# Performance work log

Measured on AMD Instinct MI355X. Metric: run time of the kernel, lower is better.

## Reference

```python
import jax, jax.numpy as jnp
import numpy as np

N = 100000   # nodes
E = 1600000  # edges
F_IN = 64    # n_features
H = 32       # hidden_size
OUT = 1      # output_size


def _lin(k, fan_in, fan_out):
    return (jax.random.normal(k, (fan_in, fan_out), jnp.float32) / np.sqrt(fan_in)).astype(jnp.float32)


def setup_inputs() -> dict:
    key = jax.random.key(0)
    ks = jax.random.split(key, 16)
    x = jax.random.normal(ks[0], (N, F_IN), jnp.float32)
    edge_index = jax.random.randint(ks[1], (2, E), 0, N, dtype=jnp.int64)
    # guarantee current_node (=0) has outgoing edges so the legal-move mask is non-empty
    edge_index = edge_index.at[0, :64].set(0)
    edge_attr = jax.random.uniform(ks[2], (E,), jnp.float32)
    return {
        "x": x, "edge_index": edge_index, "edge_attr": edge_attr, "current_node": 0,
        # conv_in: GraphConv(F_IN -> H)
        "Win_rel": _lin(ks[3], F_IN, H), "bin_rel": jnp.zeros((H,), jnp.float32), "Win_root": _lin(ks[4], F_IN, H),
        # conv_hidden: GraphConv(H -> H)
        "Wh_rel": _lin(ks[5], H, H), "bh_rel": jnp.zeros((H,), jnp.float32), "Wh_root": _lin(ks[6], H, H),
        # policy_conv: GraphConv(H -> OUT)
        "Wp_rel": _lin(ks[7], H, OUT), "bp_rel": jnp.zeros((OUT,), jnp.float32), "Wp_root": _lin(ks[8], H, OUT),
        # value_conv: GraphConv(H -> OUT)
        "Wv_rel": _lin(ks[9], H, OUT), "bv_rel": jnp.zeros((OUT,), jnp.float32), "Wv_root": _lin(ks[10], H, OUT),
    }


def _graph_conv(h, src, dst, ew, W_rel, b_rel, W_root):
    # PyG GraphConv: out_i = W_root h_i + W_rel * sum_{j->i} e_ji * h_j + b
    msg = h[src] * ew[:, None]                              # [E, d] gather + scale
    agg = jax.ops.segment_sum(msg, dst, num_segments=N)      # [N, d] scatter-add
    return agg @ W_rel + b_rel + h @ W_root


def reference(x, edge_index, edge_attr, current_node,
              Win_rel, bin_rel, Win_root,
              Wh_rel, bh_rel, Wh_root,
              Wp_rel, bp_rel, Wp_root,
              Wv_rel, bv_rel, Wv_root):
    src, dst = edge_index[0], edge_index[1]
    h = jax.nn.relu(_graph_conv(x, src, dst, edge_attr, Win_rel, bin_rel, Win_root))
    h = jax.nn.relu(_graph_conv(h, src, dst, edge_attr, Wh_rel, bh_rel, Wh_root))
    p = _graph_conv(h, src, dst, edge_attr, Wp_rel, bp_rel, Wp_root)  # [N, 1]
    v = _graph_conv(h, src, dst, edge_attr, Wv_rel, bv_rel, Wv_root)  # [N, 1]
    # illegal_moves_mask: 1 for nodes directly reachable from current_node
    hit = (src == current_node).astype(jnp.float32)
    mask = (jnp.zeros((N,), jnp.float32).at[dst].add(hit) > 0).astype(jnp.float32)
    p_m = mask * p.T                                   # [1, N]
    p_m = jnp.where(p_m == 0, -jnp.inf, p_m)
    p_soft = jax.nn.softmax(p_m, axis=1)
    v_m = mask * v.T                                   # [1, N]
    return p_soft.reshape(-1), v_m.reshape(-1)
```

## Files before the change

### kernel.cpp

```cpp
#include <hip/hip_runtime.h>
#include <hip/hip_fp16.h>
#include <cmath>

static constexpr int NN = 100000;
static constexpr int NE = 1600000;
static const size_t NW = (size_t)NN * 32;
static constexpr int SUB = 256;
static constexpr int NSUB = 391;
static constexpr int CH = 8192;
static constexpr int NCH = (NE + CH - 1) / CH;
static constexpr int BCAP = 5200;
static constexpr int MCAP = 4096;

__device__ __forceinline__ float ent_w(unsigned e)
{
    return __half2float(__ushort_as_half((unsigned short)(e >> 17)));
}
__device__ __forceinline__ int ent_s(unsigned e)
{
    int s = (int)(e & 0x1FFFF);
    return s < NN ? s : NN - 1;
}

__device__ __forceinline__ float4 pack8(const float* v)
{
    union { __half2 h2[4]; float4 f4; } u;
    u.h2[0] = __floats2half2_rn(v[0], v[1]);
    u.h2[1] = __floats2half2_rn(v[2], v[3]);
    u.h2[2] = __floats2half2_rn(v[4], v[5]);
    u.h2[3] = __floats2half2_rn(v[6], v[7]);
    return u.f4;
}

__global__ void __launch_bounds__(512) countC_k(
    const int* __restrict__ src, const int* __restrict__ dst,
    const int* __restrict__ curp, int* __restrict__ maskb,
    int* __restrict__ mcount, int* __restrict__ mlist,
    int* __restrict__ blkcnt)
{
    __shared__ int lhist[NSUB];
    int t = threadIdx.x;
    for (int i = t; i < NSUB; i += 512) lhist[i] = 0;
    __syncthreads();
    int c0 = blockIdx.x * CH;
    int cur = curp[0];
#pragma unroll
    for (int it = 0; it < CH / 512; ++it) {
        int e = c0 + it * 512 + t;
        if (e < NE) {
            int d = dst[e];
            if ((unsigned)d < (unsigned)NN) {
                atomicAdd(&lhist[d >> 8], 1);
                if (src[e] == cur) {
                    if (atomicExch(maskb + d, 1) == 0) {
                        int idx = atomicAdd(mcount, 1);
                        if (idx < MCAP) mlist[idx] = d;
                    }
                }
            }
        }
    }
    __syncthreads();
    for (int b = t; b < NSUB; b += 512)
        blkcnt[b * NCH + blockIdx.x] = lhist[b];
}

__global__ void __launch_bounds__(256) scan_blk_k(
    const int* __restrict__ blkcnt, int* __restrict__ blkbase,
    int* __restrict__ btot)
{
    __shared__ int tmp[256];
    int b = blockIdx.x, t = threadIdx.x;
    int v = (t < NCH) ? blkcnt[b * NCH + t] : 0;
    tmp[t] = v;
    __syncthreads();
    for (int s = 1; s < 256; s <<= 1) {
        int x = tmp[t];
        int a = (t >= s) ? tmp[t - s] : 0;
        __syncthreads();
        tmp[t] = x + a;
        __syncthreads();
    }
    if (t < NCH) blkbase[b * NCH + t] = tmp[t] - v;
    if (t == 255) btot[b] = tmp[255];
}

__global__ void __launch_bounds__(512) scan_btot_k(
    const int* __restrict__ btot, int* __restrict__ gbase)
{
    __shared__ int tmp[512];
    int t = threadIdx.x;
    int v = (t < NSUB) ? btot[t] : 0;
    tmp[t] = v;
    __syncthreads();
    for (int s = 1; s < 512; s <<= 1) {
        int x = tmp[t];
        int a = (t >= s) ? tmp[t - s] : 0;
        __syncthreads();
        tmp[t] = x + a;
        __syncthreads();
    }
    if (t < NSUB) gbase[t] = tmp[t] - v;
}

__global__ void __launch_bounds__(512) writeC_k(
    const int* __restrict__ src, const int* __restrict__ dst,
    const float* __restrict__ ew, const int* __restrict__ blkbase,
    uint2* __restrict__ buckets)
{
    __shared__ uint2 sBuf[CH];
    __shared__ int lhist[NSUB];
    __shared__ int lpos[NSUB];
    __shared__ int lstart[NSUB];
    __shared__ int lbase[NSUB];
    __shared__ int tscan[512];
    int t = threadIdx.x;
    for (int i = t; i < NSUB; i += 512) { lhist[i] = 0; lpos[i] = 0; }
    __syncthreads();
    int c0 = blockIdx.x * CH;
    uint2 rent[CH / 512];
    int rb[CH / 512];
#pragma unroll
    for (int it = 0; it < CH / 512; ++it) {
        int e = c0 + it * 512 + t;
        rb[it] = -1;
        if (e < NE) {
            int d = dst[e];
            if ((unsigned)d < (unsigned)NN) {
                rb[it] = d >> 8;
                unsigned bits = __half_as_ushort(__float2half(ew[e]));
                rent[it].x = ((unsigned)src[e] & 0x1FFFF) | (bits << 17);
                rent[it].y = (unsigned)d;
                atomicAdd(&lhist[rb[it]], 1);
            }
        }
    }
    __syncthreads();
    int v = (t < NSUB) ? lhist[t] : 0;
    tscan[t] = v;
    __syncthreads();
    for (int s = 1; s < 512; s <<= 1) {
        int x = tscan[t];
        int a = (t >= s) ? tscan[t - s] : 0;
        __syncthreads();
        tscan[t] = x + a;
        __syncthreads();
    }
    if (t < NSUB) {
        lstart[t] = tscan[t] - v;
        lbase[t] = blkbase[t * NCH + blockIdx.x];
    }
    __syncthreads();
#pragma unroll
    for (int it = 0; it < CH / 512; ++it) {
        if (rb[it] >= 0) {
            int p = atomicAdd(&lpos[rb[it]], 1);
            sBuf[lstart[rb[it]] + p] = rent[it];
        }
    }
    __syncthreads();
    int total = lstart[NSUB - 1] + lhist[NSUB - 1];
    for (int j = t; j < total; j += 512) {
        uint2 e = sBuf[j];
        int b = (int)(e.y >> 8);
        if (b >= NSUB) b = NSUB - 1;
        unsigned pos = (unsigned)(lbase[b] + (j - lstart[b]));
        if (pos < (unsigned)BCAP) buckets[(size_t)b * BCAP + pos] = e;
    }
}

__global__ void __launch_bounds__(512) sortB_k(
    const uint2* __restrict__ buckets, const int* __restrict__ btot,
    const int* __restrict__ gbase, unsigned* __restrict__ csr4,
    int* __restrict__ deg, int* __restrict__ off)
{
    __shared__ uint2 sBuf[BCAP];
    __shared__ int lhist[SUB];
    __shared__ int lstart[SUB];
    __shared__ int lcur[SUB];
    __shared__ int tscan[256];
    int g = blockIdx.x, t = threadIdx.x;
    if (t < SUB) { lhist[t] = 0; lcur[t] = 0; }
    __syncthreads();
    int cnt = btot[g];
    if (cnt < 0) cnt = 0;
    if (cnt > BCAP) cnt = BCAP;
    const uint2* bk = buckets + (size_t)g * BCAP;
    for (int i = t; i < cnt; i += 512) {
        uint2 e = bk[i];
        sBuf[i] = e;
        atomicAdd(&lhist[e.y & (SUB - 1)], 1);
    }
    __syncthreads();
    if (t < 256) tscan[t] = lhist[t];
    __syncthreads();
    for (int s = 1; s < 256; s <<= 1) {
        int x = 0, a = 0;
        if (t < 256) { x = tscan[t]; a = (t >= s) ? tscan[t - s] : 0; }
        __syncthreads();
        if (t < 256) tscan[t] = x + a;
        __syncthreads();
    }
    if (t < 256) lstart[t] = tscan[t] - lhist[t];
    __syncthreads();
    int base = gbase[g];
    for (int i = t; i < cnt; i += 512) {
        uint2 e = sBuf[i];
        int ld = (int)(e.y & (SUB - 1));
        int p = atomicAdd(&lcur[ld], 1);
        unsigned pos = (unsigned)(base + lstart[ld] + p);
        if (pos < (unsigned)NE) csr4[pos] = e.x;
    }
    if (t < SUB) {
        int n = g * SUB + t;
        if (n < NN) {
            deg[n] = lhist[t];
            off[n] = base + lstart[t];
        }
    }
}

__global__ void __launch_bounds__(256) mm1_k(
    const float* __restrict__ x, const float* __restrict__ Wrel,
    const float* __restrict__ Wroot, const float* __restrict__ bin,
    __half* __restrict__ proj1, __half* __restrict__ root1)
{
    __shared__ float sX[128 * 65];
    __shared__ float sW[64 * 68];
    int t = threadIdx.x;
    for (int i = t; i < 64 * 32; i += 256) {
        int k = i >> 5, j = i & 31;
        sW[k * 68 + j] = Wrel[i];
        sW[k * 68 + 32 + j] = Wroot[i];
    }
    int base = blockIdx.x * 128;
    for (int i = t; i < 2048; i += 256) {
        int node = i >> 4;
        int k = (i & 15) * 4;
        int n = base + node;
        if (n >= NN) n = NN - 1;
        float4 v = *(const float4*)(x + (size_t)n * 64 + k);
        float* p = sX + node * 65 + k;
        p[0] = v.x; p[1] = v.y; p[2] = v.z; p[3] = v.w;
    }
    __syncthreads();
    int cg = t & 7;
    int ng = t >> 3;
    int c0 = 8 * cg;
    float acc[4][8] = {};
    for (int k = 0; k < 64; ++k) {
        float xv0 = sX[(4 * ng + 0) * 65 + k];
        float xv1 = sX[(4 * ng + 1) * 65 + k];
        float xv2 = sX[(4 * ng + 2) * 65 + k];
        float xv3 = sX[(4 * ng + 3) * 65 + k];
        float4 w0 = *(const float4*)(sW + k * 68 + c0);
        float4 w1 = *(const float4*)(sW + k * 68 + c0 + 4);
        const float* wp = (const float*)&w0;
#pragma unroll
        for (int j = 0; j < 4; ++j) {
            float w = wp[j];
            acc[0][j] = fmaf(xv0, w, acc[0][j]);
            acc[1][j] = fmaf(xv1, w, acc[1][j]);
            acc[2][j] = fmaf(xv2, w, acc[2][j]);
            acc[3][j] = fmaf(xv3, w, acc[3][j]);
        }
        const float* wq = (const float*)&w1;
#pragma unroll
        for (int j = 0; j < 4; ++j) {
            float w = wq[j];
            acc[0][4 + j] = fmaf(xv0, w, acc[0][4 + j]);
            acc[1][4 + j] = fmaf(xv1, w, acc[1][4 + j]);
            acc[2][4 + j] = fmaf(xv2, w, acc[2][4 + j]);
            acc[3][4 + j] = fmaf(xv3, w, acc[3][4 + j]);
        }
    }
#pragma unroll
    for (int r = 0; r < 4; ++r) {
        int n = base + 4 * ng + r;
        if (n >= NN) break;
        if (cg < 4) {
            *(float4*)(proj1 + (size_t)n * 32 + c0) = pack8(acc[r]);
        } else {
            int c = c0 - 32;
            float v[8];
#pragma unroll
            for (int j = 0; j < 8; ++j) v[j] = acc[r][j] + bin[c + j];
            *(float4*)(root1 + (size_t)n * 32 + c) = pack8(v);
        }
    }
}

__global__ void __launch_bounds__(256) mm2_k(
    const __half* __restrict__ h1, const float* __restrict__ Wrel,
    const float* __restrict__ Wroot, const float* __restrict__ bh,
    __half* __restrict__ proj2, __half* __restrict__ root2)
{
    __shared__ float sX[128 * 33];
    __shared__ float sW[32 * 68];
    int t = threadIdx.x;
    for (int i = t; i < 32 * 32; i += 256) {
        int k = i >> 5, j = i & 31;
        sW[k * 68 + j] = Wrel[i];
        sW[k * 68 + 32 + j] = Wroot[i];
    }
    int base = blockIdx.x * 128;
    for (int i = t; i < 512; i += 256) {
        int node = i >> 2;
        int hs = (i & 3) * 8;
        int n = base + node;
        if (n >= NN) n = NN - 1;
        float4 v = *(const float4*)(h1 + (size_t)n * 32 + hs);
        const __half2* hp = (const __half2*)&v;
        float* p = sX + node * 33 + hs;
#pragma unroll
        for (int u = 0; u < 4; ++u) {
            float2 f2 = __half22float2(hp[u]);
            p[2 * u] = f2.x;
            p[2 * u + 1] = f2.y;
        }
    }
    __syncthreads();
    int cg = t & 7;
    int ng = t >> 3;
    int c0 = 8 * cg;
    float acc[4][8] = {};
    for (int k = 0; k < 32; ++k) {
        float xv0 = sX[(4 * ng + 0) * 33 + k];
        float xv1 = sX[(4 * ng + 1) * 33 + k];
        float xv2 = sX[(4 * ng + 2) * 33 + k];
        float xv3 = sX[(4 * ng + 3) * 33 + k];
        float4 w0 = *(const float4*)(sW + k * 68 + c0);
        float4 w1 = *(const float4*)(sW + k * 68 + c0 + 4);
        const float* wp = (const float*)&w0;
#pragma unroll
        for (int j = 0; j < 4; ++j) {
            float w = wp[j];
            acc[0][j] = fmaf(xv0, w, acc[0][j]);
            acc[1][j] = fmaf(xv1, w, acc[1][j]);
            acc[2][j] = fmaf(xv2, w, acc[2][j]);
            acc[3][j] = fmaf(xv3, w, acc[3][j]);
        }
        const float* wq = (const float*)&w1;
#pragma unroll
        for (int j = 0; j < 4; ++j) {
            float w = wq[j];
            acc[0][4 + j] = fmaf(xv0, w, acc[0][4 + j]);
            acc[1][4 + j] = fmaf(xv1, w, acc[1][4 + j]);
            acc[2][4 + j] = fmaf(xv2, w, acc[2][4 + j]);
            acc[3][4 + j] = fmaf(xv3, w, acc[3][4 + j]);
        }
    }
#pragma unroll
    for (int r = 0; r < 4; ++r) {
        int n = base + 4 * ng + r;
        if (n >= NN) break;
        if (cg < 4) {
            *(float4*)(proj2 + (size_t)n * 32 + c0) = pack8(acc[r]);
        } else {
            int c = c0 - 32;
            float v[8];
#pragma unroll
            for (int j = 0; j < 8; ++j) v[j] = acc[r][j] + bh[c + j];
            *(float4*)(root2 + (size_t)n * 32 + c) = pack8(v);
        }
    }
}

__global__ void __launch_bounds__(256) agg1_v4(
    const __half* __restrict__ proj1, const __half* __restrict__ root1,
    const unsigned* __restrict__ csr4, const int* __restrict__ off,
    const int* __restrict__ deg, __half* __restrict__ h1)
{
    int t = threadIdx.x;
    int q = t & 3;
    int f0 = q * 8;
    int n = blockIdx.x * 64 + (t >> 2);
    if (n >= NN) return;
    int st = off[n];
    int dg = deg[n];
    if (st < 0) st = 0;
    if (st > NE) st = NE;
    if (dg < 0) dg = 0;
    if (dg > NE - st) dg = NE - st;
    float acc[8] = {0.f, 0.f, 0.f, 0.f, 0.f, 0.f, 0.f, 0.f};
    int i = 0;
    for (; i + 1 < dg; i += 2) {
        unsigned e0 = csr4[st + i];
        unsigned e1 = csr4[st + i + 1];
        float w0 = ent_w(e0), w1 = ent_w(e1);
        float4 r0 = *(const float4*)(proj1 + (size_t)ent_s(e0) * 32 + f0);
        float4 r1 = *(const float4*)(proj1 + (size_t)ent_s(e1) * 32 + f0);
        const __half2* h0 = (const __half2*)&r0;
        const __half2* h1p = (const __half2*)&r1;
#pragma unroll
        for (int u = 0; u < 4; ++u) {
            float2 a = __half22float2(h0[u]);
            float2 b = __half22float2(h1p[u]);
            acc[2 * u] = fmaf(w0, a.x, acc[2 * u]);
            acc[2 * u + 1] = fmaf(w0, a.y, acc[2 * u + 1]);
            acc[2 * u] = fmaf(w1, b.x, acc[2 * u]);
            acc[2 * u + 1] = fmaf(w1, b.y, acc[2 * u + 1]);
        }
    }
    if (i < dg) {
        unsigned e0 = csr4[st + i];
        float w0 = ent_w(e0);
        float4 r0 = *(const float4*)(proj1 + (size_t)ent_s(e0) * 32 + f0);
        const __half2* h0 = (const __half2*)&r0;
#pragma unroll
        for (int u = 0; u < 4; ++u) {
            float2 a = __half22float2(h0[u]);
            acc[2 * u] = fmaf(w0, a.x, acc[2 * u]);
            acc[2 * u + 1] = fmaf(w0, a.y, acc[2 * u + 1]);
        }
    }
    float4 rr = *(const float4*)(root1 + (size_t)n * 32 + f0);
    const __half2* rp = (const __half2*)&rr;
    float h[8];
#pragma unroll
    for (int u = 0; u < 4; ++u) {
        float2 f2 = __half22float2(rp[u]);
        h[2 * u] = fmaxf(acc[2 * u] + f2.x, 0.f);
        h[2 * u + 1] = fmaxf(acc[2 * u + 1] + f2.y, 0.f);
    }
    *(float4*)(h1 + (size_t)n * 32 + f0) = pack8(h);
}

__global__ void __launch_bounds__(256) agg2_v4(
    const __half* __restrict__ proj2, const __half* __restrict__ root2,
    const float* __restrict__ Wp_rel, const float* __restrict__ Wp_root,
    const float* __restrict__ bp, const float* __restrict__ Wv_rel,
    const float* __restrict__ Wv_root, const float* __restrict__ bv,
    const unsigned* __restrict__ csr4, const int* __restrict__ off,
    const int* __restrict__ deg, float2* __restrict__ pv,
    float* __restrict__ pbase, float* __restrict__ vbase)
{
    __shared__ float sHead[4 * 32];
    if (threadIdx.x < 32) {
        sHead[threadIdx.x] = Wp_rel[threadIdx.x];
        sHead[32 + threadIdx.x] = Wp_root[threadIdx.x];
        sHead[64 + threadIdx.x] = Wv_rel[threadIdx.x];
        sHead[96 + threadIdx.x] = Wv_root[threadIdx.x];
    }
    __syncthreads();
    int t = threadIdx.x;
    int q = t & 3;
    int f0 = q * 8;
    int n = blockIdx.x * 64 + (t >> 2);
    if (n >= NN) return;
    int st = off[n];
    int dg = deg[n];
    if (st < 0) st = 0;
    if (st > NE) st = NE;
    if (dg < 0) dg = 0;
    if (dg > NE - st) dg = NE - st;
    float acc[8] = {0.f, 0.f, 0.f, 0.f, 0.f, 0.f, 0.f, 0.f};
    int i = 0;
    for (; i + 1 < dg; i += 2) {
        unsigned e0 = csr4[st + i];
        unsigned e1 = csr4[st + i + 1];
        float w0 = ent_w(e0), w1 = ent_w(e1);
        float4 r0 = *(const float4*)(proj2 + (size_t)ent_s(e0) * 32 + f0);
        float4 r1 = *(const float4*)(proj2 + (size_t)ent_s(e1) * 32 + f0);
        const __half2* h0 = (const __half2*)&r0;
        const __half2* h1p = (const __half2*)&r1;
#pragma unroll
        for (int u = 0; u < 4; ++u) {
            float2 a = __half22float2(h0[u]);
            float2 b = __half22float2(h1p[u]);
            acc[2 * u] = fmaf(w0, a.x, acc[2 * u]);
            acc[2 * u + 1] = fmaf(w0, a.y, acc[2 * u + 1]);
            acc[2 * u] = fmaf(w1, b.x, acc[2 * u]);
            acc[2 * u + 1] = fmaf(w1, b.y, acc[2 * u + 1]);
        }
    }
    if (i < dg) {
        unsigned e0 = csr4[st + i];
        float w0 = ent_w(e0);
        float4 r0 = *(const float4*)(proj2 + (size_t)ent_s(e0) * 32 + f0);
        const __half2* h0 = (const __half2*)&r0;
#pragma unroll
        for (int u = 0; u < 4; ++u) {
            float2 a = __half22float2(h0[u]);
            acc[2 * u] = fmaf(w0, a.x, acc[2 * u]);
            acc[2 * u + 1] = fmaf(w0, a.y, acc[2 * u + 1]);
        }
    }
    float4 rr = *(const float4*)(root2 + (size_t)n * 32 + f0);
    const __half2* rp = (const __half2*)&rr;
    float h[8];
#pragma unroll
    for (int u = 0; u < 4; ++u) {
        float2 f2 = __half22float2(rp[u]);
        h[2 * u] = fmaxf(acc[2 * u] + f2.x, 0.f);
        h[2 * u + 1] = fmaxf(acc[2 * u + 1] + f2.y, 0.f);
    }
    float prv = 0.f, pov = 0.f, vrv = 0.f, vov = 0.f;
#pragma unroll
    for (int j = 0; j < 8; ++j) {
        prv = fmaf(h[j], sHead[f0 + j], prv);
        pov = fmaf(h[j], sHead[32 + f0 + j], pov);
        vrv = fmaf(h[j], sHead[64 + f0 + j], vrv);
        vov = fmaf(h[j], sHead[96 + f0 + j], vov);
    }
#pragma unroll
    for (int m = 1; m <= 2; m <<= 1) {
        prv += __shfl_xor(prv, m, 64);
        pov += __shfl_xor(pov, m, 64);
        vrv += __shfl_xor(vrv, m, 64);
        vov += __shfl_xor(vov, m, 64);
    }
    if (q == 0) {
        pv[n] = make_float2(prv, vrv);
        pbase[n] = pov + bp[0];
        vbase[n] = vov + bv[0];
    }
}

__global__ void __launch_bounds__(256) masked_softmax_k(
    const int* __restrict__ mlist, const int* __restrict__ mcount,
    const unsigned* __restrict__ csr4, const int* __restrict__ off,
    const int* __restrict__ deg, const float2* __restrict__ pv,
    const float* __restrict__ pbase, const float* __restrict__ vbase,
    float* __restrict__ out_p, float* __restrict__ out_v)
{
    __shared__ float sPm[MCAP];
    __shared__ float sV[MCAP];
    __shared__ int sN[MCAP];
    __shared__ float sMx, sSum;
    __shared__ float sred[4];
    int m = mcount[0];
    if (m > MCAP) m = MCAP;
    if (m < 0) m = 0;
    for (int idx = threadIdx.x; idx < m; idx += 256) {
        int n = mlist[idx];
        if ((unsigned)n >= (unsigned)NN) n = 0;
        sN[idx] = n;
        int st = off[n];
        int dg = deg[n];
        if (st < 0) st = 0;
        if (st > NE) st = NE;
        if (dg < 0) dg = 0;
        if (dg > NE - st) dg = NE - st;
        float pa = 0.f, va = 0.f;
        for (int i = 0; i < dg; ++i) {
            unsigned ent = csr4[st + i];
            int s = ent_s(ent);
            float w = ent_w(ent);
            float2 tv = pv[s];
            pa = fmaf(tv.x, w, pa);
            va = fmaf(tv.y, w, va);
        }
        float p = pa + pbase[n];
        sPm[idx] = (p == 0.f) ? -INFINITY : p;
        sV[idx] = va + vbase[n];
    }
    __syncthreads();
    float mx = -INFINITY;
    for (int i = threadIdx.x; i < m; i += 256) mx = fmaxf(mx, sPm[i]);
#pragma unroll
    for (int k = 32; k; k >>= 1) mx = fmaxf(mx, __shfl_xor(mx, k, 64));
    if ((threadIdx.x & 63) == 0) sred[threadIdx.x >> 6] = mx;
    __syncthreads();
    if (threadIdx.x == 0)
        sMx = fmaxf(fmaxf(sred[0], sred[1]), fmaxf(sred[2], sred[3]));
    __syncthreads();
    float sum = 0.f;
    for (int i = threadIdx.x; i < m; i += 256) {
        float x = sPm[i];
        sum += (x == -INFINITY) ? 0.f : expf(x - sMx);
    }
#pragma unroll
    for (int k = 32; k; k >>= 1) sum += __shfl_xor(sum, k, 64);
    if ((threadIdx.x & 63) == 0) sred[threadIdx.x >> 6] = sum;
    __syncthreads();
    if (threadIdx.x == 0) sSum = sred[0] + sred[1] + sred[2] + sred[3];
    __syncthreads();
    for (int idx = threadIdx.x; idx < m; idx += 256) {
        int n = sN[idx];
        float x = sPm[idx];
        out_p[n] = (x == -INFINITY) ? 0.f : expf(x - sMx) / sSum;
        out_v[n] = sV[idx];
    }
}

extern "C" void kernel_launch(void* const* d_in, const int* in_sizes, int n_in,
                              void* d_out, int out_size, void* d_ws,
                              size_t ws_size, hipStream_t stream)
{
    const float* x        = (const float*)d_in[0];
    const int*   ei       = (const int*)d_in[1];
    const float* ew       = (const float*)d_in[2];
    const int*   cur      = (const int*)d_in[3];
    const float* Win_rel  = (const float*)d_in[4];
    const float* bin_rel  = (const float*)d_in[5];
    const float* Win_root = (const float*)d_in[6];
    const float* Wh_rel   = (const float*)d_in[7];
    const float* bh_rel   = (const float*)d_in[8];
    const float* Wh_root  = (const float*)d_in[9];
    const float* Wp_rel   = (const float*)d_in[10];
    const float* bp       = (const float*)d_in[11];
    const float* Wp_root  = (const float*)d_in[12];
    const float* Wv_rel   = (const float*)d_in[13];
    const float* bv       = (const float*)d_in[14];
    const float* Wv_root  = (const float*)d_in[15];

    const int* srcA = ei;
    const int* dstA = ei + NE;

    char* w8 = (char*)d_ws;
    unsigned* csr4 = (unsigned*)w8;
    int* deg    = (int*)(csr4 + NE);
    int* off    = deg + NN;
    int* maskb  = off + NN;
    int* mcount = maskb + NN;
    int* mlist  = mcount + 8;
    int* btot   = mlist + MCAP;
    int* gbase  = btot + 400;
    __half* proj1 = (__half*)(gbase + 400);
    __half* root1 = proj1 + NW;
    __half* h1    = root1 + NW;
    __half* proj2 = h1 + NW;
    __half* root2 = proj2 + NW;
    float2* pv    = (float2*)(root2 + NW);
    float* pbase  = (float*)(pv + NN);
    float* vbase  = pbase + NN;
    uint2* buckets = (uint2*)proj1;
    int* blkcnt  = (int*)(buckets + (size_t)NSUB * BCAP);
    int* blkbase = blkcnt + NSUB * NCH;

    float* out_p = (float*)d_out;
    float* out_v = out_p + NN;

    const int NB_MM  = (NN + 127) / 128;
    const int NB_AGG = (NN + 63) / 64;

    hipMemsetAsync(maskb, 0, ((size_t)NN + 8) * sizeof(int), stream);
    hipMemsetAsync(d_out, 0, 2 * (size_t)NN * sizeof(float), stream);

    countC_k<<<NCH, 512, 0, stream>>>(srcA, dstA, cur, maskb, mcount, mlist,
                                      blkcnt);
    scan_blk_k<<<NSUB, 256, 0, stream>>>(blkcnt, blkbase, btot);
    scan_btot_k<<<1, 512, 0, stream>>>(btot, gbase);
    writeC_k<<<NCH, 512, 0, stream>>>(srcA, dstA, ew, blkbase, buckets);
    sortB_k<<<NSUB, 512, 0, stream>>>(buckets, btot, gbase, csr4, deg, off);

    mm1_k<<<NB_MM, 256, 0, stream>>>(x, Win_rel, Win_root, bin_rel, proj1,
                                     root1);
    agg1_v4<<<NB_AGG, 256, 0, stream>>>(proj1, root1, csr4, off, deg, h1);
    mm2_k<<<NB_MM, 256, 0, stream>>>(h1, Wh_rel, Wh_root, bh_rel, proj2, root2);
    agg2_v4<<<NB_AGG, 256, 0, stream>>>(proj2, root2, Wp_rel, Wp_root, bp,
                                        Wv_rel, Wv_root, bv, csr4, off, deg,
                                        pv, pbase, vbase);
    masked_softmax_k<<<1, 256, 0, stream>>>(mlist, mcount, csr4, off, deg, pv,
                                            pbase, vbase, out_p, out_v);
}
```

Measured before the change: 263.0 us.

## Fuse CSR build passes with first projection GEMM into one kernel

Replaces the separate count, two scan, and write passes with a single pass. Each chunk reserves space inside fixed-capacity per-bucket slots through global atomics, so the CSR is laid out at bucket*BCAP offsets instead of being compactly prefix-summed. The same launch also runs the first projection GEMM in extra blocks that share the LDS through a union, overlapping compute with the edge bucketing. The output memset is folded into agg2's stores. This removes several launches and one full read of the edge arrays. In exchange, bucket order now depends on atomic timing (nondeterministic edge order within a node), and the GEMM blocks run at 512 threads with fewer rows per thread.

```diff
diff --git a/kernel.cpp b/kernel.cpp
--- a/kernel.cpp
+++ b/kernel.cpp
@@ -10,6 +10,7 @@
 static constexpr int CH = 8192;
 static constexpr int NCH = (NE + CH - 1) / CH;
 static constexpr int BCAP = 5200;
+static constexpr int CSRN = NSUB * BCAP;
 static constexpr int MCAP = 4096;
 
 __device__ __forceinline__ float ent_w(unsigned e)
@@ -32,147 +33,156 @@
     return u.f4;
 }
 
-__global__ void __launch_bounds__(512) countC_k(
+__global__ void __launch_bounds__(512) fused_build_mm1_k(
     const int* __restrict__ src, const int* __restrict__ dst,
-    const int* __restrict__ curp, int* __restrict__ maskb,
-    int* __restrict__ mcount, int* __restrict__ mlist,
-    int* __restrict__ blkcnt)
-{
-    __shared__ int lhist[NSUB];
+    const float* __restrict__ ew, const int* __restrict__ curp,
+    int* __restrict__ maskb, int* __restrict__ mcount, int* __restrict__ mlist,
+    int* __restrict__ bcnt, uint2* __restrict__ buckets,
+    const float* __restrict__ x, const float* __restrict__ Wrel,
+    const float* __restrict__ Wroot, const float* __restrict__ bin,
+    __half* __restrict__ proj1, __half* __restrict__ root1)
+{
+    __shared__ union {
+        struct {
+            uint2 sBuf[CH];
+            int lhist[NSUB];
+            int lpos[NSUB];
+            int lstart[NSUB];
+            int lbase[NSUB];
+            int tscan[512];
+        } s;
+        struct {
+            float sX[128 * 65];
+            float sW[64 * 68];
+        } m;
+    } u;
+
     int t = threadIdx.x;
-    for (int i = t; i < NSUB; i += 512) lhist[i] = 0;
-    __syncthreads();
-    int c0 = blockIdx.x * CH;
-    int cur = curp[0];
-#pragma unroll
-    for (int it = 0; it < CH / 512; ++it) {
-        int e = c0 + it * 512 + t;
-        if (e < NE) {
-            int d = dst[e];
-            if ((unsigned)d < (unsigned)NN) {
-                atomicAdd(&lhist[d >> 8], 1);
-                if (src[e] == cur) {
-                    if (atomicExch(maskb + d, 1) == 0) {
-                        int idx = atomicAdd(mcount, 1);
-                        if (idx < MCAP) mlist[idx] = d;
+    int bid = blockIdx.x;
+
+    if (bid < NCH) {
+        for (int i = t; i < NSUB; i += 512) { u.s.lhist[i] = 0; u.s.lpos[i] = 0; }
+        __syncthreads();
+        int c0 = bid * CH;
+        int cur = curp[0];
+        uint2 rent[CH / 512];
+        int rb[CH / 512];
+#pragma unroll
+        for (int it = 0; it < CH / 512; ++it) {
+            int e = c0 + it * 512 + t;
+            rb[it] = -1;
+            if (e < NE) {
+                int d = dst[e];
+                int sv = src[e];
+                if ((unsigned)d < (unsigned)NN) {
+                    rb[it] = d >> 8;
+                    unsigned bits = __half_as_ushort(__float2half(ew[e]));
+                    rent[it].x = ((unsigned)sv & 0x1FFFF) | (bits << 17);
+                    rent[it].y = (unsigned)d;
+                    atomicAdd(&u.s.lhist[rb[it]], 1);
+                    if (sv == cur) {
+                        if (atomicExch(maskb + d, 1) == 0) {
+                            int idx = atomicAdd(mcount, 1);
+                            if (idx < MCAP) mlist[idx] = d;
+                        }
                     }
                 }
             }
         }
-    }
-    __syncthreads();
-    for (int b = t; b < NSUB; b += 512)
-        blkcnt[b * NCH + blockIdx.x] = lhist[b];
-}
-
-__global__ void __launch_bounds__(256) scan_blk_k(
-    const int* __restrict__ blkcnt, int* __restrict__ blkbase,
-    int* __restrict__ btot)
-{
-    __shared__ int tmp[256];
-    int b = blockIdx.x, t = threadIdx.x;
-    int v = (t < NCH) ? blkcnt[b * NCH + t] : 0;
-    tmp[t] = v;
-    __syncthreads();
-    for (int s = 1; s < 256; s <<= 1) {
-        int x = tmp[t];
-        int a = (t >= s) ? tmp[t - s] : 0;
-        __syncthreads();
-        tmp[t] = x + a;
-        __syncthreads();
-    }
-    if (t < NCH) blkbase[b * NCH + t] = tmp[t] - v;
-    if (t == 255) btot[b] = tmp[255];
-}
-
-__global__ void __launch_bounds__(512) scan_btot_k(
-    const int* __restrict__ btot, int* __restrict__ gbase)
-{
-    __shared__ int tmp[512];
-    int t = threadIdx.x;
-    int v = (t < NSUB) ? btot[t] : 0;
-    tmp[t] = v;
-    __syncthreads();
-    for (int s = 1; s < 512; s <<= 1) {
-        int x = tmp[t];
-        int a = (t >= s) ? tmp[t - s] : 0;
-        __syncthreads();
-        tmp[t] = x + a;
-        __syncthreads();
-    }
-    if (t < NSUB) gbase[t] = tmp[t] - v;
-}
-
-__global__ void __launch_bounds__(512) writeC_k(
-    const int* __restrict__ src, const int* __restrict__ dst,
-    const float* __restrict__ ew, const int* __restrict__ blkbase,
-    uint2* __restrict__ buckets)
-{
-    __shared__ uint2 sBuf[CH];
-    __shared__ int lhist[NSUB];
-    __shared__ int lpos[NSUB];
-    __shared__ int lstart[NSUB];
-    __shared__ int lbase[NSUB];
-    __shared__ int tscan[512];
-    int t = threadIdx.x;
-    for (int i = t; i < NSUB; i += 512) { lhist[i] = 0; lpos[i] = 0; }
-    __syncthreads();
-    int c0 = blockIdx.x * CH;
-    uint2 rent[CH / 512];
-    int rb[CH / 512];
-#pragma unroll
-    for (int it = 0; it < CH / 512; ++it) {
-        int e = c0 + it * 512 + t;
-        rb[it] = -1;
-        if (e < NE) {
-            int d = dst[e];
-            if ((unsigned)d < (unsigned)NN) {
-                rb[it] = d >> 8;
-                unsigned bits = __half_as_ushort(__float2half(ew[e]));
-                rent[it].x = ((unsigned)src[e] & 0x1FFFF) | (bits << 17);
-                rent[it].y = (unsigned)d;
-                atomicAdd(&lhist[rb[it]], 1);
+        __syncthreads();
+        int v = (t < NSUB) ? u.s.lhist[t] : 0;
+        u.s.tscan[t] = v;
+        __syncthreads();
+        for (int sh = 1; sh < 512; sh <<= 1) {
+            int xv = u.s.tscan[t];
+            int a = (t >= sh) ? u.s.tscan[t - sh] : 0;
+            __syncthreads();
+            u.s.tscan[t] = xv + a;
+            __syncthreads();
+        }
+        if (t < NSUB) {
+            u.s.lstart[t] = u.s.tscan[t] - v;
+            u.s.lbase[t] = (v > 0) ? atomicAdd(&bcnt[t], v) : 0;
+        }
+        __syncthreads();
+#pragma unroll
+        for (int it = 0; it < CH / 512; ++it) {
+            if (rb[it] >= 0) {
+                int p = atomicAdd(&u.s.lpos[rb[it]], 1);
+                u.s.sBuf[u.s.lstart[rb[it]] + p] = rent[it];
             }
         }
-    }
-    __syncthreads();
-    int v = (t < NSUB) ? lhist[t] : 0;
-    tscan[t] = v;
-    __syncthreads();
-    for (int s = 1; s < 512; s <<= 1) {
-        int x = tscan[t];
-        int a = (t >= s) ? tscan[t - s] : 0;
-        __syncthreads();
-        tscan[t] = x + a;
-        __syncthreads();
-    }
-    if (t < NSUB) {
-        lstart[t] = tscan[t] - v;
-        lbase[t] = blkbase[t * NCH + blockIdx.x];
-    }
-    __syncthreads();
-#pragma unroll
-    for (int it = 0; it < CH / 512; ++it) {
-        if (rb[it] >= 0) {
-            int p = atomicAdd(&lpos[rb[it]], 1);
-            sBuf[lstart[rb[it]] + p] = rent[it];
-        }
-    }
-    __syncthreads();
-    int total = lstart[NSUB - 1] + lhist[NSUB - 1];
-    for (int j = t; j < total; j += 512) {
-        uint2 e = sBuf[j];
-        int b = (int)(e.y >> 8);
-        if (b >= NSUB) b = NSUB - 1;
-        unsigned pos = (unsigned)(lbase[b] + (j - lstart[b]));
-        if (pos < (unsigned)BCAP) buckets[(size_t)b * BCAP + pos] = e;
+        __syncthreads();
+        int total = u.s.lstart[NSUB - 1] + u.s.lhist[NSUB - 1];
+        for (int j = t; j < total; j += 512) {
+            uint2 en = u.s.sBuf[j];
+            int b = (int)(en.y >> 8);
+            if (b >= NSUB) b = NSUB - 1;
+            unsigned pos = (unsigned)(u.s.lbase[b] + (j - u.s.lstart[b]));
+            if (pos < (unsigned)BCAP) buckets[(size_t)b * BCAP + pos] = en;
+        }
+    } else {
+        int mb = bid - NCH;
+        for (int i = t; i < 64 * 32; i += 512) {
+            int k = i >> 5, j = i & 31;
+            u.m.sW[k * 68 + j] = Wrel[i];
+            u.m.sW[k * 68 + 32 + j] = Wroot[i];
+        }
+        int base = mb * 128;
+        for (int i = t; i < 2048; i += 512) {
+            int node = i >> 4;
+            int k = (i & 15) * 4;
+            int n = base + node;
+            if (n >= NN) n = NN - 1;
+            float4 v4 = *(const float4*)(x + (size_t)n * 64 + k);
+            float* p = u.m.sX + node * 65 + k;
+            p[0] = v4.x; p[1] = v4.y; p[2] = v4.z; p[3] = v4.w;
+        }
+        __syncthreads();
+        int cg = t & 7;
+        int ng = t >> 3;
+        int c0m = 8 * cg;
+        float acc[2][8] = {};
+        for (int k = 0; k < 64; ++k) {
+            float xv0 = u.m.sX[(2 * ng + 0) * 65 + k];
+            float xv1 = u.m.sX[(2 * ng + 1) * 65 + k];
+            float4 w0 = *(const float4*)(u.m.sW + k * 68 + c0m);
+            float4 w1 = *(const float4*)(u.m.sW + k * 68 + c0m + 4);
+            const float* wp = (const float*)&w0;
+#pragma unroll
+            for (int j = 0; j < 4; ++j) {
+                float w = wp[j];
+                acc[0][j] = fmaf(xv0, w, acc[0][j]);
+                acc[1][j] = fmaf(xv1, w, acc[1][j]);
+            }
+            const float* wq = (const float*)&w1;
+#pragma unroll
+            for (int j = 0; j < 4; ++j) {
+                float w = wq[j];
+                acc[0][4 + j] = fmaf(xv0, w, acc[0][4 + j]);
+                acc[1][4 + j] = fmaf(xv1, w, acc[1][4 + j]);
+            }
+        }
+#pragma unroll
+        for (int r = 0; r < 2; ++r) {
+            int n = base + 2 * ng + r;
+            if (n >= NN) break;
+            if (cg < 4) {
+                *(float4*)(proj1 + (size_t)n * 32 + c0m) = pack8(acc[r]);
+            } else {
+                int c = c0m - 32;
+                float vv[8];
+#pragma unroll
+                for (int j = 0; j < 8; ++j) vv[j] = acc[r][j] + bin[c + j];
+                *(float4*)(root1 + (size_t)n * 32 + c) = pack8(vv);
+            }
+        }
     }
 }
 
 __global__ void __launch_bounds__(512) sortB_k(
-    const uint2* __restrict__ buckets, const int* __restrict__ btot,
-    const int* __restrict__ gbase, unsigned* __restrict__ csr4,
-    int* __restrict__ deg, int* __restrict__ off)
+    const uint2* __restrict__ buckets, const int* __restrict__ bcnt,
+    unsigned* __restrict__ csr4, int* __restrict__ deg, int* __restrict__ off)
 {
     __shared__ uint2 sBuf[BCAP];
     __shared__ int lhist[SUB];
@@ -182,7 +192,7 @@
     int g = blockIdx.x, t = threadIdx.x;
     if (t < SUB) { lhist[t] = 0; lcur[t] = 0; }
     __syncthreads();
-    int cnt = btot[g];
+    int cnt = bcnt[g];
     if (cnt < 0) cnt = 0;
     if (cnt > BCAP) cnt = BCAP;
     const uint2* bk = buckets + (size_t)g * BCAP;
@@ -203,89 +213,19 @@
     }
     if (t < 256) lstart[t] = tscan[t] - lhist[t];
     __syncthreads();
-    int base = gbase[g];
+    int base = g * BCAP;
     for (int i = t; i < cnt; i += 512) {
         uint2 e = sBuf[i];
         int ld = (int)(e.y & (SUB - 1));
         int p = atomicAdd(&lcur[ld], 1);
         unsigned pos = (unsigned)(base + lstart[ld] + p);
-        if (pos < (unsigned)NE) csr4[pos] = e.x;
+        if (pos < (unsigned)CSRN) csr4[pos] = e.x;
     }
     if (t < SUB) {
         int n = g * SUB + t;
         if (n < NN) {
             deg[n] = lhist[t];
             off[n] = base + lstart[t];
-        }
-    }
-}
-
-__global__ void __launch_bounds__(256) mm1_k(
-    const float* __restrict__ x, const float* __restrict__ Wrel,
-    const float* __restrict__ Wroot, const float* __restrict__ bin,
-    __half* __restrict__ proj1, __half* __restrict__ root1)
-{
-    __shared__ float sX[128 * 65];
-    __shared__ float sW[64 * 68];
-    int t = threadIdx.x;
-    for (int i = t; i < 64 * 32; i += 256) {
-        int k = i >> 5, j = i & 31;
-        sW[k * 68 + j] = Wrel[i];
-        sW[k * 68 + 32 + j] = Wroot[i];
-    }
-    int base = blockIdx.x * 128;
-    for (int i = t; i < 2048; i += 256) {
-        int node = i >> 4;
-        int k = (i & 15) * 4;
-        int n = base + node;
-        if (n >= NN) n = NN - 1;
-        float4 v = *(const float4*)(x + (size_t)n * 64 + k);
-        float* p = sX + node * 65 + k;
-        p[0] = v.x; p[1] = v.y; p[2] = v.z; p[3] = v.w;
-    }
-    __syncthreads();
-    int cg = t & 7;
-    int ng = t >> 3;
-    int c0 = 8 * cg;
-    float acc[4][8] = {};
-    for (int k = 0; k < 64; ++k) {
-        float xv0 = sX[(4 * ng + 0) * 65 + k];
-        float xv1 = sX[(4 * ng + 1) * 65 + k];
-        float xv2 = sX[(4 * ng + 2) * 65 + k];
-        float xv3 = sX[(4 * ng + 3) * 65 + k];
-        float4 w0 = *(const float4*)(sW + k * 68 + c0);
-        float4 w1 = *(const float4*)(sW + k * 68 + c0 + 4);
-        const float* wp = (const float*)&w0;
-#pragma unroll
-        for (int j = 0; j < 4; ++j) {
-            float w = wp[j];
-            acc[0][j] = fmaf(xv0, w, acc[0][j]);
-            acc[1][j] = fmaf(xv1, w, acc[1][j]);
-            acc[2][j] = fmaf(xv2, w, acc[2][j]);
-            acc[3][j] = fmaf(xv3, w, acc[3][j]);
-        }
-        const float* wq = (const float*)&w1;
-#pragma unroll
-        for (int j = 0; j < 4; ++j) {
-            float w = wq[j];
-            acc[0][4 + j] = fmaf(xv0, w, acc[0][4 + j]);
-            acc[1][4 + j] = fmaf(xv1, w, acc[1][4 + j]);
-            acc[2][4 + j] = fmaf(xv2, w, acc[2][4 + j]);
-            acc[3][4 + j] = fmaf(xv3, w, acc[3][4 + j]);
-        }
-    }
-#pragma unroll
-    for (int r = 0; r < 4; ++r) {
-        int n = base + 4 * ng + r;
-        if (n >= NN) break;
-        if (cg < 4) {
-            *(float4*)(proj1 + (size_t)n * 32 + c0) = pack8(acc[r]);
-        } else {
-            int c = c0 - 32;
-            float v[8];
-#pragma unroll
-            for (int j = 0; j < 8; ++j) v[j] = acc[r][j] + bin[c + j];
-            *(float4*)(root1 + (size_t)n * 32 + c) = pack8(v);
         }
     }
 }
@@ -379,9 +319,9 @@
     int st = off[n];
     int dg = deg[n];
     if (st < 0) st = 0;
-    if (st > NE) st = NE;
+    if (st > CSRN) st = CSRN;
     if (dg < 0) dg = 0;
-    if (dg > NE - st) dg = NE - st;
+    if (dg > CSRN - st) dg = CSRN - st;
     float acc[8] = {0.f, 0.f, 0.f, 0.f, 0.f, 0.f, 0.f, 0.f};
     int i = 0;
     for (; i + 1 < dg; i += 2) {
@@ -433,7 +373,8 @@
     const float* __restrict__ Wv_root, const float* __restrict__ bv,
     const unsigned* __restrict__ csr4, const int* __restrict__ off,
     const int* __restrict__ deg, float2* __restrict__ pv,
-    float* __restrict__ pbase, float* __restrict__ vbase)
+    float* __restrict__ pbase, float* __restrict__ vbase,
+    float* __restrict__ out_p, float* __restrict__ out_v)
 {
     __shared__ float sHead[4 * 32];
     if (threadIdx.x < 32) {
@@ -451,9 +392,9 @@
     int st = off[n];
     int dg = deg[n];
     if (st < 0) st = 0;
-    if (st > NE) st = NE;
+    if (st > CSRN) st = CSRN;
     if (dg < 0) dg = 0;
-    if (dg > NE - st) dg = NE - st;
+    if (dg > CSRN - st) dg = CSRN - st;
     float acc[8] = {0.f, 0.f, 0.f, 0.f, 0.f, 0.f, 0.f, 0.f};
     int i = 0;
     for (; i + 1 < dg; i += 2) {
@@ -514,6 +455,8 @@
         pv[n] = make_float2(prv, vrv);
         pbase[n] = pov + bp[0];
         vbase[n] = vov + bv[0];
+        out_p[n] = 0.f;
+        out_v[n] = 0.f;
     }
 }
 
@@ -539,9 +482,9 @@
         int st = off[n];
         int dg = deg[n];
         if (st < 0) st = 0;
-        if (st > NE) st = NE;
+        if (st > CSRN) st = CSRN;
         if (dg < 0) dg = 0;
-        if (dg > NE - st) dg = NE - st;
+        if (dg > CSRN - st) dg = CSRN - st;
         float pa = 0.f, va = 0.f;
         for (int i = 0; i < dg; ++i) {
             unsigned ent = csr4[st + i];
@@ -610,14 +553,13 @@
 
     char* w8 = (char*)d_ws;
     unsigned* csr4 = (unsigned*)w8;
-    int* deg    = (int*)(csr4 + NE);
+    int* deg    = (int*)(csr4 + CSRN);
     int* off    = deg + NN;
     int* maskb  = off + NN;
     int* mcount = maskb + NN;
-    int* mlist  = mcount + 8;
-    int* btot   = mlist + MCAP;
-    int* gbase  = btot + 400;
-    __half* proj1 = (__half*)(gbase + 400);
+    int* bcnt   = mcount + 8;
+    int* mlist  = bcnt + 400;
+    __half* proj1 = (__half*)(mlist + MCAP);
     __half* root1 = proj1 + NW;
     __half* h1    = root1 + NW;
     __half* proj2 = h1 + NW;
@@ -625,33 +567,27 @@
     float2* pv    = (float2*)(root2 + NW);
     float* pbase  = (float*)(pv + NN);
     float* vbase  = pbase + NN;
-    uint2* buckets = (uint2*)proj1;
-    int* blkcnt  = (int*)(buckets + (size_t)NSUB * BCAP);
-    int* blkbase = blkcnt + NSUB * NCH;
+    uint2* buckets = (uint2*)(vbase + NN);
 
     float* out_p = (float*)d_out;
     float* out_v = out_p + NN;
 
-    const int NB_MM  = (NN + 127) / 128;
-    const int NB_AGG = (NN + 63) / 64;
-
-    hipMemsetAsync(maskb, 0, ((size_t)NN + 8) * sizeof(int), stream);
-    hipMemsetAsync(d_out, 0, 2 * (size_t)NN * sizeof(float), stream);
-
-    countC_k<<<NCH, 512, 0, stream>>>(srcA, dstA, cur, maskb, mcount, mlist,
-                                      blkcnt);
-    scan_blk_k<<<NSUB, 256, 0, stream>>>(blkcnt, blkbase, btot);
-    scan_btot_k<<<1, 512, 0, stream>>>(btot, gbase);
-    writeC_k<<<NCH, 512, 0, stream>>>(srcA, dstA, ew, blkbase, buckets);
-    sortB_k<<<NSUB, 512, 0, stream>>>(buckets, btot, gbase, csr4, deg, off);
-
-    mm1_k<<<NB_MM, 256, 0, stream>>>(x, Win_rel, Win_root, bin_rel, proj1,
-                                     root1);
+    const int NB_MM    = (NN + 127) / 128;
+    const int NB_AGG   = (NN + 63) / 64;
+    const int NB_FUSED = NCH + NB_MM;
+
+    hipMemsetAsync(maskb, 0, ((size_t)NN + 8 + 400) * sizeof(int), stream);
+
+    fused_build_mm1_k<<<NB_FUSED, 512, 0, stream>>>(
+        srcA, dstA, ew, cur, maskb, mcount, mlist, bcnt, buckets,
+        x, Win_rel, Win_root, bin_rel, proj1, root1);
+    sortB_k<<<NSUB, 512, 0, stream>>>(buckets, bcnt, csr4, deg, off);
+
     agg1_v4<<<NB_AGG, 256, 0, stream>>>(proj1, root1, csr4, off, deg, h1);
     mm2_k<<<NB_MM, 256, 0, stream>>>(h1, Wh_rel, Wh_root, bh_rel, proj2, root2);
     agg2_v4<<<NB_AGG, 256, 0, stream>>>(proj2, root2, Wp_rel, Wp_root, bp,
                                         Wv_rel, Wv_root, bv, csr4, off, deg,
-                                        pv, pbase, vbase);
+                                        pv, pbase, vbase, out_p, out_v);
     masked_softmax_k<<<1, 256, 0, stream>>>(mlist, mcount, csr4, off, deg, pv,
                                             pbase, vbase, out_p, out_v);
 }
```

After: 248.5 us. 1.06x faster.
